# Optimization experiments

Measured on AMD Instinct MI355X. Metric: run time of the kernel, lower is better.

Reference implementation:

```python
import jax, jax.numpy as jnp
import numpy as np

B, S, D_MODEL, D_K, D_V = 4, 2048, 1024, 1024, 1024


def setup_inputs() -> dict:
    key = jax.random.key(0)
    k1, k2, k3, k4 = jax.random.split(key, 4)
    scale = 1.0 / np.sqrt(D_MODEL)
    x = jax.random.normal(k1, (B, S, D_MODEL), dtype=jnp.float32)
    Wq = jax.random.normal(k2, (D_K, D_MODEL), dtype=jnp.float32) * scale
    Wk = jax.random.normal(k3, (D_K, D_MODEL), dtype=jnp.float32) * scale
    Wv = jax.random.normal(k4, (D_V, D_MODEL), dtype=jnp.float32) * scale
    # causal mask: position i may attend to j <= i (True = keep)
    mask = jnp.broadcast_to(jnp.tril(jnp.ones((S, S), dtype=bool)), (B, S, S))
    return {"x": x, "mask": mask, "Wq": Wq, "Wk": Wk, "Wv": Wv}


def reference(x, mask, Wq, Wk, Wv):
    # nn.Linear(d, k, bias=False): y = x @ W.T with W of shape [k, d]
    q = jnp.einsum('bsd,kd->bsk', x, Wq)
    k = jnp.einsum('bsd,kd->bsk', x, Wk)
    v = jnp.einsum('bsd,vd->bsv', x, Wv)
    scores = jnp.einsum('bik,bjk->bij', q, k) / jnp.sqrt(jnp.float32(D_K))
    s = jnp.where(mask, scores, -jnp.inf)
    # masked, fully-masked-row-safe softmax (fully masked rows -> all zeros,
    # matching softmax[all-masked rows] = 0 in the original)
    m = jnp.max(s, axis=-1, keepdims=True)
    m_safe = jnp.where(jnp.isfinite(m), m, 0.0)
    e = jnp.exp(s - m_safe)          # exp(-inf) = 0 for masked entries
    denom = jnp.sum(e, axis=-1, keepdims=True)
    p = e / jnp.where(denom == 0.0, 1.0, denom)
    return jnp.einsum('bij,bjv->biv', p, v)
```

## Files before the change

kernel.cpp:

```cpp
#include <hip/hip_runtime.h>
#include <hip/hip_bf16.h>
#include <stdint.h>

#define SEQ   2048
#define DM    1024
#define NBAT  4

typedef __attribute__((ext_vector_type(8))) short  short8;
typedef __attribute__((ext_vector_type(4))) float  floatx4;

__device__ __forceinline__ unsigned short f2b(float f) {
    __hip_bfloat16 h = __float2bfloat16(f);
    unsigned short r;
    __builtin_memcpy(&r, &h, 2);
    return r;
}

__device__ __forceinline__ ushort4 pack4(float a, float b, float c, float d) {
    ushort4 u; u.x = f2b(a); u.y = f2b(b); u.z = f2b(c); u.w = f2b(d); return u;
}

__device__ __forceinline__ void gload16(const void* g, void* s) {
    __builtin_amdgcn_global_load_lds(
        (const __attribute__((address_space(1))) unsigned int*)(uintptr_t)g,
        (__attribute__((address_space(3))) unsigned int*)(uintptr_t)s,
        16, 0, 0);
}

__global__ void prep(const float4* __restrict__ x,
                     const float4* __restrict__ w0, const float4* __restrict__ w1,
                     const float4* __restrict__ w2,
                     ushort4* __restrict__ xb, ushort4* __restrict__ wall,
                     float* __restrict__ rsum)
{
    const int b = blockIdx.x;
    const int t = threadIdx.x;
    if (b < 8192) {
        const int i = b * 256 + t;
        float4 f = x[i];
        xb[i] = pack4(f.x, f.y, f.z, f.w);
    } else if (b < 11264) {
        const int idx  = b - 8192;
        const int wsel = idx >> 10;
        const int i    = (idx & 1023) * 256 + t;
        const float4* src = (wsel == 0) ? w0 : (wsel == 1) ? w1 : w2;
        float4 f = src[i];
        wall[(size_t)wsel * 262144 + i] = pack4(f.x, f.y, f.z, f.w);
    } else {
        rsum[(b - 11264) * 256 + t] = 0.f;
    }
}

#define SLOTS 24576

__global__ __launch_bounds__(512, 2) void qkv_gemm(
    const unsigned short* __restrict__ A, const unsigned short* __restrict__ Bm,
    unsigned short* __restrict__ Qo, unsigned short* __restrict__ Ko,
    unsigned short* __restrict__ Vto, float qscale)
{
    __shared__ __align__(16) unsigned short lds[3 * SLOTS];

    const int bid = blockIdx.x;
    const int wg  = (bid & 7) * 96 + (bid >> 3);
    const int mt  = wg / 24, nt = wg - mt * 24;
    const int m0  = mt * 256, n0 = nt * 128;

    const int t    = threadIdx.x;
    const int w    = t >> 6;
    const int lane = t & 63;
    const int wr   = w >> 1, wc = w & 1;
    const int r    = lane & 15, q = lane >> 4;

    const int srow = lane >> 3;
    const int scol = ((lane & 7) ^ srow) << 3;

    const int aoff = (wr >> 1) * 8192 + ((wr & 1) * 64 + r) * 64;
    const int boff = 16384 + (wc * 64 + r) * 64;
    const int sk0  = ((0 + q) ^ (r & 7)) * 8;
    const int sk1  = ((4 + q) ^ (r & 7)) * 8;

    floatx4 acc[4][4];
#pragma unroll
    for (int i = 0; i < 4; i++)
#pragma unroll
        for (int j = 0; j < 4; j++)
            acc[i][j] = (floatx4){0.f, 0.f, 0.f, 0.f};

#define STGA(KB, SL) do { \
    gload16(A + (((size_t)(m0 +       w * 16 + srow)) << 10) + (KB) + scol, &lds[(SL) +         w * 1024]); \
    gload16(A + (((size_t)(m0 +   8 + w * 16 + srow)) << 10) + (KB) + scol, &lds[(SL) +         w * 1024 + 512]); \
    gload16(A + (((size_t)(m0 + 128 + w * 16 + srow)) << 10) + (KB) + scol, &lds[(SL) + 8192 +  w * 1024]); \
    gload16(A + (((size_t)(m0 + 136 + w * 16 + srow)) << 10) + (KB) + scol, &lds[(SL) + 8192 +  w * 1024 + 512]); \
  } while (0)
#define STGB(KB, SL) do { \
    gload16(Bm + (((size_t)(n0 +      w * 16 + srow)) << 10) + (KB) + scol, &lds[(SL) + 16384 + w * 1024]); \
    gload16(Bm + (((size_t)(n0 +  8 + w * 16 + srow)) << 10) + (KB) + scol, &lds[(SL) + 16384 + w * 1024 + 512]); \
  } while (0)

#define MFMA16() do { \
    acc[0][0] = __builtin_amdgcn_mfma_f32_16x16x32_bf16(af0, bf0, acc[0][0], 0, 0, 0); \
    acc[0][1] = __builtin_amdgcn_mfma_f32_16x16x32_bf16(af0, bf1, acc[0][1], 0, 0, 0); \
    acc[0][2] = __builtin_amdgcn_mfma_f32_16x16x32_bf16(af0, bf2, acc[0][2], 0, 0, 0); \
    acc[0][3] = __builtin_amdgcn_mfma_f32_16x16x32_bf16(af0, bf3, acc[0][3], 0, 0, 0); \
    acc[1][0] = __builtin_amdgcn_mfma_f32_16x16x32_bf16(af1, bf0, acc[1][0], 0, 0, 0); \
    acc[1][1] = __builtin_amdgcn_mfma_f32_16x16x32_bf16(af1, bf1, acc[1][1], 0, 0, 0); \
    acc[1][2] = __builtin_amdgcn_mfma_f32_16x16x32_bf16(af1, bf2, acc[1][2], 0, 0, 0); \
    acc[1][3] = __builtin_amdgcn_mfma_f32_16x16x32_bf16(af1, bf3, acc[1][3], 0, 0, 0); \
    acc[2][0] = __builtin_amdgcn_mfma_f32_16x16x32_bf16(af2, bf0, acc[2][0], 0, 0, 0); \
    acc[2][1] = __builtin_amdgcn_mfma_f32_16x16x32_bf16(af2, bf1, acc[2][1], 0, 0, 0); \
    acc[2][2] = __builtin_amdgcn_mfma_f32_16x16x32_bf16(af2, bf2, acc[2][2], 0, 0, 0); \
    acc[2][3] = __builtin_amdgcn_mfma_f32_16x16x32_bf16(af2, bf3, acc[2][3], 0, 0, 0); \
    acc[3][0] = __builtin_amdgcn_mfma_f32_16x16x32_bf16(af3, bf0, acc[3][0], 0, 0, 0); \
    acc[3][1] = __builtin_amdgcn_mfma_f32_16x16x32_bf16(af3, bf1, acc[3][1], 0, 0, 0); \
    acc[3][2] = __builtin_amdgcn_mfma_f32_16x16x32_bf16(af3, bf2, acc[3][2], 0, 0, 0); \
    acc[3][3] = __builtin_amdgcn_mfma_f32_16x16x32_bf16(af3, bf3, acc[3][3], 0, 0, 0); \
  } while (0)

    STGA(0, 0);
    STGB(0, 0);
    STGA(64, SLOTS);
    STGB(64, SLOTS);
    asm volatile("s_waitcnt vmcnt(6)" ::: "memory");
    __builtin_amdgcn_s_barrier();

    short8 af0, af1, af2, af3, bf0, bf1, bf2, bf3;

    for (int tt = 0; tt < 16; ++tt) {
        const int sl  = (tt % 3) * SLOTS;
        const int nsl = ((tt + 2) % 3) * SLOTS;
        const int nkb = (tt + 2 < 16) ? (tt + 2) * 64 : 0;

        {
            const int aB = sl + aoff + sk0;
            const int bB = sl + boff + sk0;
            af0 = *(const short8*)&lds[aB +    0];
            af1 = *(const short8*)&lds[aB + 1024];
            af2 = *(const short8*)&lds[aB + 2048];
            af3 = *(const short8*)&lds[aB + 3072];
            bf0 = *(const short8*)&lds[bB +    0];
            bf1 = *(const short8*)&lds[bB + 1024];
            bf2 = *(const short8*)&lds[bB + 2048];
            bf3 = *(const short8*)&lds[bB + 3072];
            STGA(nkb, nsl);
            __builtin_amdgcn_s_barrier();
            asm volatile("s_waitcnt lgkmcnt(0)" ::: "memory");
            __builtin_amdgcn_s_setprio(1);
            MFMA16();
            __builtin_amdgcn_s_setprio(0);
            __builtin_amdgcn_s_barrier();
        }
        {
            const int aB = sl + aoff + sk1;
            const int bB = sl + boff + sk1;
            af0 = *(const short8*)&lds[aB +    0];
            af1 = *(const short8*)&lds[aB + 1024];
            af2 = *(const short8*)&lds[aB + 2048];
            af3 = *(const short8*)&lds[aB + 3072];
            bf0 = *(const short8*)&lds[bB +    0];
            bf1 = *(const short8*)&lds[bB + 1024];
            bf2 = *(const short8*)&lds[bB + 2048];
            bf3 = *(const short8*)&lds[bB + 3072];
            STGB(nkb, nsl);
            asm volatile("s_waitcnt vmcnt(6)" ::: "memory");
            __builtin_amdgcn_s_barrier();
            asm volatile("s_waitcnt lgkmcnt(0)" ::: "memory");
            __builtin_amdgcn_s_setprio(1);
            MFMA16();
            __builtin_amdgcn_s_setprio(0);
            __builtin_amdgcn_s_barrier();
        }
    }
#undef STGA
#undef STGB
#undef MFMA16

    const int gmb = m0 + wr * 64 + q * 4;
    const int gnb = n0 + wc * 64 + r;
    if (nt < 8) {
#pragma unroll
        for (int i = 0; i < 4; i++) {
            const int gm = gmb + i * 16;
#pragma unroll
            for (int j = 0; j < 4; j++) {
                const int gn = gnb + j * 16;
#pragma unroll
                for (int rr = 0; rr < 4; rr++)
                    Qo[(size_t)(gm + rr) * 1024 + gn] = f2b(acc[i][j][rr] * qscale);
            }
        }
    } else if (nt < 16) {
#pragma unroll
        for (int i = 0; i < 4; i++) {
            const int gm = gmb + i * 16;
#pragma unroll
            for (int j = 0; j < 4; j++) {
                const int gn = gnb + j * 16;
#pragma unroll
                for (int rr = 0; rr < 4; rr++)
                    Ko[(size_t)(gm + rr) * 1024 + (gn - 1024)] = f2b(acc[i][j][rr]);
            }
        }
    } else {
#pragma unroll
        for (int i = 0; i < 4; i++) {
            const int gm = gmb + i * 16;
            const int b  = gm >> 11;
            const int s  = gm & 2047;
#pragma unroll
            for (int j = 0; j < 4; j++) {
                const int v = gnb + j * 16 - 2048;
                *(ushort4*)&Vto[((size_t)(b * 1024 + v)) * 2048 + s] =
                    pack4(acc[i][j][0], acc[i][j][1], acc[i][j][2], acc[i][j][3]);
            }
        }
    }
}

template<int MODE>
__global__ __launch_bounds__(256) void attn64(
    const unsigned short* __restrict__ Ag, const unsigned short* __restrict__ Bg,
    void* __restrict__ Cv, float* __restrict__ rowsum)
{
    const int z = blockIdx.z;
    int m0, n0;
    if (MODE == 0) {
        const int f = blockIdx.x;
        int ti = (int)((sqrtf(4.f * f + 1.f) - 1.f) * 0.5f);
        while ((ti + 1) * (ti + 2) <= f) ti++;
        while (ti * (ti + 1) > f) ti--;
        const int tj = f - ti * (ti + 1);
        m0 = ti * 128;
        n0 = tj * 64;
    } else {
        m0 = (int)(gridDim.y - 1 - blockIdx.y) * 128;
        n0 = blockIdx.x * 64;
    }

    const int lda = (MODE == 0) ? DM : SEQ;
    const int ldb = (MODE == 0) ? DM : SEQ;
    const unsigned short* A  = Ag + (size_t)z * ((MODE == 0) ? SEQ * DM : SEQ * SEQ);
    const unsigned short* Bm = Bg + (size_t)z * ((MODE == 0) ? SEQ * DM : DM * SEQ);
    const int kEnd = (MODE == 0) ? DM : (m0 + 128);

    __shared__ __align__(16) unsigned short As[128 * 64];
    __shared__ __align__(16) unsigned short Bs[64 * 64];

    const int t    = threadIdx.x;
    const int w    = t >> 6;
    const int lane = t & 63;
    const int r    = lane & 15, q = lane >> 4;

    floatx4 acc[2][4];
#pragma unroll
    for (int i = 0; i < 2; i++)
#pragma unroll
        for (int j = 0; j < 4; j++)
            acc[i][j] = (floatx4){0.f, 0.f, 0.f, 0.f};

    const int rr0 = t >> 3;
    const int pg  = (t & 7) ^ ((t >> 3) & 7);
    const int swz = r & 7;

    for (int k0 = 0; k0 < kEnd; k0 += 64) {
        const size_t ka = (size_t)k0 + pg * 8;
#pragma unroll
        for (int g = 0; g < 4; g++)
            gload16(A + (size_t)(m0 + g * 32 + rr0) * lda + ka,
                    As + g * 2048 + (size_t)w * 512);
#pragma unroll
        for (int g = 0; g < 2; g++)
            gload16(Bm + (size_t)(n0 + g * 32 + rr0) * ldb + ka,
                    Bs + g * 2048 + (size_t)w * 512);
        __builtin_amdgcn_s_waitcnt(0);
        __syncthreads();

#pragma unroll
        for (int kk = 0; kk < 2; kk++) {
            short8 af[2], bf[4];
            const int slot = ((kk * 4 + q) ^ swz) * 8;
#pragma unroll
            for (int i = 0; i < 2; i++)
                af[i] = *(const short8*)&As[(w * 32 + i * 16 + r) * 64 + slot];
#pragma unroll
            for (int j = 0; j < 4; j++)
                bf[j] = *(const short8*)&Bs[(j * 16 + r) * 64 + slot];
#pragma unroll
            for (int i = 0; i < 2; i++)
#pragma unroll
                for (int j = 0; j < 4; j++)
                    acc[i][j] = __builtin_amdgcn_mfma_f32_16x16x32_bf16(bf[j], af[i], acc[i][j], 0, 0, 0);
        }
        __syncthreads();
    }

    const int gmb = m0 + w * 32 + r;
    const int gnb = n0 + q * 4;
    if (MODE == 0) {
        unsigned short* E = (unsigned short*)Cv + (size_t)z * SEQ * SEQ;
        float* rs = rowsum + (size_t)z * SEQ;
#pragma unroll
        for (int i = 0; i < 2; i++) {
            const int gm = gmb + i * 16;
            float part = 0.f;
#pragma unroll
            for (int j = 0; j < 4; j++) {
                const int gn = gnb + j * 16;
                float e0 = (gn + 0 <= gm) ? __expf(acc[i][j][0]) : 0.f;
                float e1 = (gn + 1 <= gm) ? __expf(acc[i][j][1]) : 0.f;
                float e2 = (gn + 2 <= gm) ? __expf(acc[i][j][2]) : 0.f;
                float e3 = (gn + 3 <= gm) ? __expf(acc[i][j][3]) : 0.f;
                part += (e0 + e1) + (e2 + e3);
                *(ushort4*)&E[(size_t)gm * SEQ + gn] = pack4(e0, e1, e2, e3);
            }
            part += __shfl_xor(part, 16, 64);
            part += __shfl_xor(part, 32, 64);
            if (q == 0) atomicAdd(&rs[gm], part);
        }
    } else {
        float* C = (float*)Cv + (size_t)z * SEQ * DM;
        const float* rs = rowsum + (size_t)z * SEQ;
#pragma unroll
        for (int i = 0; i < 2; i++) {
            const int gm = gmb + i * 16;
            const float inv = 1.0f / rs[gm];
#pragma unroll
            for (int j = 0; j < 4; j++) {
                const int gn = gnb + j * 16;
                float4 o;
                o.x = acc[i][j][0] * inv;
                o.y = acc[i][j][1] * inv;
                o.z = acc[i][j][2] * inv;
                o.w = acc[i][j][3] * inv;
                *(float4*)&C[(size_t)gm * DM + gn] = o;
            }
        }
    }
}

extern "C" void kernel_launch(void* const* d_in, const int* in_sizes, int n_in,
                              void* d_out, int out_size, void* d_ws, size_t ws_size,
                              hipStream_t stream) {
    (void)in_sizes; (void)n_in; (void)out_size; (void)ws_size;
    const float* x  = (const float*)d_in[0];
    const float* Wq = (const float*)d_in[2];
    const float* Wk = (const float*)d_in[3];
    const float* Wv = (const float*)d_in[4];

    char* base = (char*)d_ws;
    size_t off = 0;
    auto alloc = [&](size_t n) { char* p = base + off; off += (n + 255) & ~(size_t)255; return p; };

    unsigned short* xb   = (unsigned short*)alloc((size_t)NBAT * SEQ * DM * 2);
    unsigned short* wall = (unsigned short*)alloc((size_t)3 * DM * DM * 2);
    unsigned short* Qb   = (unsigned short*)alloc((size_t)NBAT * SEQ * DM * 2);
    unsigned short* Kb   = (unsigned short*)alloc((size_t)NBAT * SEQ * DM * 2);
    unsigned short* Vtb  = (unsigned short*)alloc((size_t)NBAT * DM * SEQ * 2);
    unsigned short* E    = (unsigned short*)alloc((size_t)NBAT * SEQ * SEQ * 2);
    float*          rsum = (float*)alloc((size_t)NBAT * SEQ * 4);

    const dim3 blk(256);

    prep<<<dim3(11296), blk, 0, stream>>>(
        (const float4*)x, (const float4*)Wq, (const float4*)Wk, (const float4*)Wv,
        (ushort4*)xb, (ushort4*)wall, rsum);

    qkv_gemm<<<dim3(768), dim3(512), 0, stream>>>(
        xb, wall, Qb, Kb, Vtb, 0.03125f);

    attn64<0><<<dim3(272, 1, NBAT), blk, 0, stream>>>(Qb, Kb, E, rsum);

    attn64<1><<<dim3(DM / 64, SEQ / 128, NBAT), blk, 0, stream>>>(E, Vtb, d_out, rsum);
}
```

Baseline: 267.4 us.

## Enlarge attention GEMM tiles to 256x128 with triple-buffered LDS pipeline

```diff
diff --git a/kernel.cpp b/kernel.cpp
--- a/kernel.cpp
+++ b/kernel.cpp
@@ -217,10 +217,12 @@
 }
 
 template<int MODE>
-__global__ __launch_bounds__(256) void attn64(
+__global__ __launch_bounds__(512, 2) void attn256(
     const unsigned short* __restrict__ Ag, const unsigned short* __restrict__ Bg,
     void* __restrict__ Cv, float* __restrict__ rowsum)
 {
+    __shared__ __align__(16) unsigned short lds[3 * SLOTS];
+
     const int z = blockIdx.z;
     int m0, n0;
     if (MODE == 0) {
@@ -229,77 +231,135 @@
         while ((ti + 1) * (ti + 2) <= f) ti++;
         while (ti * (ti + 1) > f) ti--;
         const int tj = f - ti * (ti + 1);
-        m0 = ti * 128;
-        n0 = tj * 64;
+        m0 = ti * 256;
+        n0 = tj * 128;
     } else {
-        m0 = (int)(gridDim.y - 1 - blockIdx.y) * 128;
-        n0 = blockIdx.x * 64;
-    }
-
-    const int lda = (MODE == 0) ? DM : SEQ;
-    const int ldb = (MODE == 0) ? DM : SEQ;
+        m0 = (int)(gridDim.y - 1 - blockIdx.y) * 256;
+        n0 = blockIdx.x * 128;
+    }
+
+    const size_t LDA = (MODE == 0) ? DM : SEQ;
+    const size_t LDB = (MODE == 0) ? DM : SEQ;
     const unsigned short* A  = Ag + (size_t)z * ((MODE == 0) ? SEQ * DM : SEQ * SEQ);
     const unsigned short* Bm = Bg + (size_t)z * ((MODE == 0) ? SEQ * DM : DM * SEQ);
-    const int kEnd = (MODE == 0) ? DM : (m0 + 128);
-
-    __shared__ __align__(16) unsigned short As[128 * 64];
-    __shared__ __align__(16) unsigned short Bs[64 * 64];
+    const int NT = ((MODE == 0) ? DM : (m0 + 256)) / 64;
 
     const int t    = threadIdx.x;
     const int w    = t >> 6;
     const int lane = t & 63;
+    const int wr   = w >> 1, wc = w & 1;
     const int r    = lane & 15, q = lane >> 4;
 
-    floatx4 acc[2][4];
-#pragma unroll
-    for (int i = 0; i < 2; i++)
+    const int srow = lane >> 3;
+    const int scol = ((lane & 7) ^ srow) << 3;
+
+    const int aoff = (wr >> 1) * 8192 + ((wr & 1) * 64 + r) * 64;
+    const int boff = 16384 + (wc * 64 + r) * 64;
+    const int sk0  = ((0 + q) ^ (r & 7)) * 8;
+    const int sk1  = ((4 + q) ^ (r & 7)) * 8;
+
+    floatx4 acc[4][4];
+#pragma unroll
+    for (int i = 0; i < 4; i++)
 #pragma unroll
         for (int j = 0; j < 4; j++)
             acc[i][j] = (floatx4){0.f, 0.f, 0.f, 0.f};
 
-    const int rr0 = t >> 3;
-    const int pg  = (t & 7) ^ ((t >> 3) & 7);
-    const int swz = r & 7;
-
-    for (int k0 = 0; k0 < kEnd; k0 += 64) {
-        const size_t ka = (size_t)k0 + pg * 8;
-#pragma unroll
-        for (int g = 0; g < 4; g++)
-            gload16(A + (size_t)(m0 + g * 32 + rr0) * lda + ka,
-                    As + g * 2048 + (size_t)w * 512);
-#pragma unroll
-        for (int g = 0; g < 2; g++)
-            gload16(Bm + (size_t)(n0 + g * 32 + rr0) * ldb + ka,
-                    Bs + g * 2048 + (size_t)w * 512);
-        __builtin_amdgcn_s_waitcnt(0);
-        __syncthreads();
-
-#pragma unroll
-        for (int kk = 0; kk < 2; kk++) {
-            short8 af[2], bf[4];
-            const int slot = ((kk * 4 + q) ^ swz) * 8;
-#pragma unroll
-            for (int i = 0; i < 2; i++)
-                af[i] = *(const short8*)&As[(w * 32 + i * 16 + r) * 64 + slot];
-#pragma unroll
-            for (int j = 0; j < 4; j++)
-                bf[j] = *(const short8*)&Bs[(j * 16 + r) * 64 + slot];
-#pragma unroll
-            for (int i = 0; i < 2; i++)
-#pragma unroll
-                for (int j = 0; j < 4; j++)
-                    acc[i][j] = __builtin_amdgcn_mfma_f32_16x16x32_bf16(bf[j], af[i], acc[i][j], 0, 0, 0);
-        }
-        __syncthreads();
-    }
-
-    const int gmb = m0 + w * 32 + r;
-    const int gnb = n0 + q * 4;
+#define ASTG(KB, SL) do { \
+    gload16(A + (size_t)(m0 +       w * 16 + srow) * LDA + (KB) + scol, &lds[(SL) +         w * 1024]); \
+    gload16(A + (size_t)(m0 +   8 + w * 16 + srow) * LDA + (KB) + scol, &lds[(SL) +         w * 1024 + 512]); \
+    gload16(A + (size_t)(m0 + 128 + w * 16 + srow) * LDA + (KB) + scol, &lds[(SL) + 8192 +  w * 1024]); \
+    gload16(A + (size_t)(m0 + 136 + w * 16 + srow) * LDA + (KB) + scol, &lds[(SL) + 8192 +  w * 1024 + 512]); \
+  } while (0)
+#define BSTG(KB, SL) do { \
+    gload16(Bm + (size_t)(n0 +      w * 16 + srow) * LDB + (KB) + scol, &lds[(SL) + 16384 + w * 1024]); \
+    gload16(Bm + (size_t)(n0 +  8 + w * 16 + srow) * LDB + (KB) + scol, &lds[(SL) + 16384 + w * 1024 + 512]); \
+  } while (0)
+
+#define MFMA16S() do { \
+    acc[0][0] = __builtin_amdgcn_mfma_f32_16x16x32_bf16(bf0, af0, acc[0][0], 0, 0, 0); \
+    acc[0][1] = __builtin_amdgcn_mfma_f32_16x16x32_bf16(bf1, af0, acc[0][1], 0, 0, 0); \
+    acc[0][2] = __builtin_amdgcn_mfma_f32_16x16x32_bf16(bf2, af0, acc[0][2], 0, 0, 0); \
+    acc[0][3] = __builtin_amdgcn_mfma_f32_16x16x32_bf16(bf3, af0, acc[0][3], 0, 0, 0); \
+    acc[1][0] = __builtin_amdgcn_mfma_f32_16x16x32_bf16(bf0, af1, acc[1][0], 0, 0, 0); \
+    acc[1][1] = __builtin_amdgcn_mfma_f32_16x16x32_bf16(bf1, af1, acc[1][1], 0, 0, 0); \
+    acc[1][2] = __builtin_amdgcn_mfma_f32_16x16x32_bf16(bf2, af1, acc[1][2], 0, 0, 0); \
+    acc[1][3] = __builtin_amdgcn_mfma_f32_16x16x32_bf16(bf3, af1, acc[1][3], 0, 0, 0); \
+    acc[2][0] = __builtin_amdgcn_mfma_f32_16x16x32_bf16(bf0, af2, acc[2][0], 0, 0, 0); \
+    acc[2][1] = __builtin_amdgcn_mfma_f32_16x16x32_bf16(bf1, af2, acc[2][1], 0, 0, 0); \
+    acc[2][2] = __builtin_amdgcn_mfma_f32_16x16x32_bf16(bf2, af2, acc[2][2], 0, 0, 0); \
+    acc[2][3] = __builtin_amdgcn_mfma_f32_16x16x32_bf16(bf3, af2, acc[2][3], 0, 0, 0); \
+    acc[3][0] = __builtin_amdgcn_mfma_f32_16x16x32_bf16(bf0, af3, acc[3][0], 0, 0, 0); \
+    acc[3][1] = __builtin_amdgcn_mfma_f32_16x16x32_bf16(bf1, af3, acc[3][1], 0, 0, 0); \
+    acc[3][2] = __builtin_amdgcn_mfma_f32_16x16x32_bf16(bf2, af3, acc[3][2], 0, 0, 0); \
+    acc[3][3] = __builtin_amdgcn_mfma_f32_16x16x32_bf16(bf3, af3, acc[3][3], 0, 0, 0); \
+  } while (0)
+
+    ASTG(0, 0);
+    BSTG(0, 0);
+    ASTG(64, SLOTS);
+    BSTG(64, SLOTS);
+    asm volatile("s_waitcnt vmcnt(6)" ::: "memory");
+    __builtin_amdgcn_s_barrier();
+
+    short8 af0, af1, af2, af3, bf0, bf1, bf2, bf3;
+
+    for (int tt = 0; tt < NT; ++tt) {
+        const int sl  = (tt % 3) * SLOTS;
+        const int nsl = ((tt + 2) % 3) * SLOTS;
+        const int nkb = (tt + 2 < NT) ? (tt + 2) * 64 : 0;
+
+        {
+            const int aB = sl + aoff + sk0;
+            const int bB = sl + boff + sk0;
+            af0 = *(const short8*)&lds[aB +    0];
+            af1 = *(const short8*)&lds[aB + 1024];
+            af2 = *(const short8*)&lds[aB + 2048];
+            af3 = *(const short8*)&lds[aB + 3072];
+            bf0 = *(const short8*)&lds[bB +    0];
+            bf1 = *(const short8*)&lds[bB + 1024];
+            bf2 = *(const short8*)&lds[bB + 2048];
+            bf3 = *(const short8*)&lds[bB + 3072];
+            ASTG(nkb, nsl);
+            __builtin_amdgcn_s_barrier();
+            asm volatile("s_waitcnt lgkmcnt(0)" ::: "memory");
+            __builtin_amdgcn_s_setprio(1);
+            MFMA16S();
+            __builtin_amdgcn_s_setprio(0);
+            __builtin_amdgcn_s_barrier();
+        }
+        {
+            const int aB = sl + aoff + sk1;
+            const int bB = sl + boff + sk1;
+            af0 = *(const short8*)&lds[aB +    0];
+            af1 = *(const short8*)&lds[aB + 1024];
+            af2 = *(const short8*)&lds[aB + 2048];
+            af3 = *(const short8*)&lds[aB + 3072];
+            bf0 = *(const short8*)&lds[bB +    0];
+            bf1 = *(const short8*)&lds[bB + 1024];
+            bf2 = *(const short8*)&lds[bB + 2048];
+            bf3 = *(const short8*)&lds[bB + 3072];
+            BSTG(nkb, nsl);
+            asm volatile("s_waitcnt vmcnt(6)" ::: "memory");
+            __builtin_amdgcn_s_barrier();
+            asm volatile("s_waitcnt lgkmcnt(0)" ::: "memory");
+            __builtin_amdgcn_s_setprio(1);
+            MFMA16S();
+            __builtin_amdgcn_s_setprio(0);
+            __builtin_amdgcn_s_barrier();
+        }
+    }
+#undef ASTG
+#undef BSTG
+#undef MFMA16S
+
+    const int gmb = m0 + wr * 64 + r;
+    const int gnb = n0 + wc * 64 + q * 4;
     if (MODE == 0) {
         unsigned short* E = (unsigned short*)Cv + (size_t)z * SEQ * SEQ;
         float* rs = rowsum + (size_t)z * SEQ;
 #pragma unroll
-        for (int i = 0; i < 2; i++) {
+        for (int i = 0; i < 4; i++) {
             const int gm = gmb + i * 16;
             float part = 0.f;
 #pragma unroll
@@ -320,7 +380,7 @@
         float* C = (float*)Cv + (size_t)z * SEQ * DM;
         const float* rs = rowsum + (size_t)z * SEQ;
 #pragma unroll
-        for (int i = 0; i < 2; i++) {
+        for (int i = 0; i < 4; i++) {
             const int gm = gmb + i * 16;
             const float inv = 1.0f / rs[gm];
 #pragma unroll
@@ -358,16 +418,14 @@
     unsigned short* E    = (unsigned short*)alloc((size_t)NBAT * SEQ * SEQ * 2);
     float*          rsum = (float*)alloc((size_t)NBAT * SEQ * 4);
 
-    const dim3 blk(256);
-
-    prep<<<dim3(11296), blk, 0, stream>>>(
+    prep<<<dim3(11296), dim3(256), 0, stream>>>(
         (const float4*)x, (const float4*)Wq, (const float4*)Wk, (const float4*)Wv,
         (ushort4*)xb, (ushort4*)wall, rsum);
 
     qkv_gemm<<<dim3(768), dim3(512), 0, stream>>>(
         xb, wall, Qb, Kb, Vtb, 0.03125f);
 
-    attn64<0><<<dim3(272, 1, NBAT), blk, 0, stream>>>(Qb, Kb, E, rsum);
-
-    attn64<1><<<dim3(DM / 64, SEQ / 128, NBAT), blk, 0, stream>>>(E, Vtb, d_out, rsum);
-}
+    attn256<0><<<dim3(72, 1, NBAT), dim3(512), 0, stream>>>(Qb, Kb, E, rsum);
+
+    attn256<1><<<dim3(DM / 128, SEQ / 256, NBAT), dim3(512), 0, stream>>>(E, Vtb, d_out, rsum);
+}
```

Result: slower. 274.4 us (+2.6%).
